# Optimization experiments

Measured on AMD Instinct MI355X. Metric: run time of the kernel, lower is better.

Reference implementation:

```python
import jax, jax.numpy as jnp
import numpy as np
import math

D_MODEL = 768
N_HEADS = 12
B, L = 2, 2048
ALPHA = 0.3

def setup_inputs() -> dict:
    key = jax.random.key(0)
    ks = jax.random.split(key, 7)
    s = 0.02
    return {
        "x": jax.random.normal(ks[0], (B, L, D_MODEL), dtype=jnp.float32),
        "Wqkv_w": jax.random.normal(ks[1], (D_MODEL, 3 * D_MODEL), dtype=jnp.float32) * s,
        "Wqkv_b": jax.random.normal(ks[2], (3 * D_MODEL,), dtype=jnp.float32) * s,
        "sel_w": jax.random.normal(ks[3], (D_MODEL, 2), dtype=jnp.float32) * s,
        "sel_b": jax.random.normal(ks[4], (2,), dtype=jnp.float32) * s,
        "out_w": jax.random.normal(ks[5], (D_MODEL, D_MODEL), dtype=jnp.float32) * s,
        "out_b": jax.random.normal(ks[6], (D_MODEL,), dtype=jnp.float32) * s,
        "temperature": jnp.ones((1,), dtype=jnp.float32) * (math.sqrt(D_MODEL) * ALPHA),
    }

def reference(x, Wqkv_w, Wqkv_b, sel_w, sel_b, out_w, out_b, temperature):
    b, l, d = x.shape
    h = N_HEADS
    hd = d // h
    # QKV projection: (B, L, 3, H, hd)
    qkv = (x @ Wqkv_w + Wqkv_b).reshape(b, l, 3, h, hd)
    q, k_, v = qkv[:, :, 0], qkv[:, :, 1], qkv[:, :, 2]
    scale = 1.0 / math.sqrt(hd)
    scores = jnp.einsum('bthd,bshd->bhts', q, k_ * scale)  # (B,H,L,L)
    causal_mask = jnp.triu(jnp.full((l, l), -10000.0, dtype=scores.dtype), 1)
    attn = jax.nn.softmax(scores + causal_mask, axis=-1)
    ctx = jnp.einsum('bhts,bshd->bthd', attn, v).reshape(b, l, d)
    attn_output = ctx @ out_w + out_b  # (B,L,D)
    # selection gate: softmax over 2 logits, keep prob of class 1 -> (B,L,1)
    selection = jax.nn.softmax((x @ sel_w + sel_b) / temperature, axis=-1)[..., 1:]
    # eval-mode top-k routing
    k_sel = int(math.ceil(math.sqrt(l)))
    _, idx = jax.lax.top_k(selection[..., 0], k_sel)  # (B, k)
    gated = attn_output * selection  # (B,L,D)
    src = jnp.take_along_axis(gated, idx[..., None], axis=1)  # (B,k,D)
    y = jax.vmap(lambda xb, ib, sb: xb.at[ib].add(sb))(x, idx, src)
    return y
```

## Files before the change

### kernel.cpp

```cpp
#include <hip/hip_runtime.h>
#include <hip/hip_bf16.h>
#include <cstddef>

#define BATCH 2
#define SEQ   2048
#define DM    768
#define NH    12
#define HD    64
#define N3    2304
#define NKV   1536
#define KSEL  46
#define NROW  (BATCH*KSEL)
#define NCHUNK 32

typedef unsigned short ushort_t;
typedef __attribute__((ext_vector_type(8))) short bf16x8;
typedef __attribute__((ext_vector_type(4))) float f32x4;

__device__ __forceinline__ ushort_t f2bf(float f) {
  union { __hip_bfloat16 h; ushort_t u; } cv;
  cv.h = __float2bfloat16(f);
  return cv.u;
}
__device__ __forceinline__ float bf2f(ushort_t u) {
  union { unsigned int i; float f; } cv;
  cv.i = ((unsigned int)u) << 16;
  return cv.f;
}

#define GLD16(g, l)                                                         \
  __builtin_amdgcn_global_load_lds(                                         \
      (const __attribute__((address_space(1))) void*)(g),                   \
      (__attribute__((address_space(3))) void*)(l), 16, 0, 0)

__global__ __launch_bounds__(256) void prep_kernel(
    const float* __restrict__ x, const float* __restrict__ W,
    const float* __restrict__ Wo,
    const float* __restrict__ sel_w, const float* __restrict__ sel_b,
    const float* __restrict__ temp,
    ushort_t* __restrict__ xb, ushort_t* __restrict__ Wt,
    ushort_t* __restrict__ WoT,
    float* __restrict__ sel, float* __restrict__ y) {
  const int bx = blockIdx.x;
  const int tid = threadIdx.x;
  if (bx < 3072) {
    int i = bx * 256 + tid;
    float4 f = ((const float4*)x)[i];
    ushort4 o;
    o.x = f2bf(f.x); o.y = f2bf(f.y); o.z = f2bf(f.z); o.w = f2bf(f.w);
    ((ushort4*)xb)[i] = o;
  } else if (bx < 4800) {
    __shared__ float tile[32][33];
    const int bx2 = bx - 3072;
    const int n0 = (bx2 % 72) * 32, k0 = (bx2 / 72) * 32;
    const int r = tid >> 3, c4 = (tid & 7) * 4;
    float4 f = *(const float4*)&W[(size_t)(k0 + r) * N3 + n0 + c4];
    tile[r][c4] = f.x; tile[r][c4 + 1] = f.y; tile[r][c4 + 2] = f.z; tile[r][c4 + 3] = f.w;
    __syncthreads();
    ushort4 o;
    o.x = f2bf(tile[c4 + 0][r]);
    o.y = f2bf(tile[c4 + 1][r]);
    o.z = f2bf(tile[c4 + 2][r]);
    o.w = f2bf(tile[c4 + 3][r]);
    *(ushort4*)&Wt[(size_t)(n0 + r) * DM + k0 + c4] = o;
  } else if (bx < 5376) {
    __shared__ float tile2[32][33];
    const int bx3 = bx - 4800;
    const int n0 = (bx3 % 24) * 32, k0 = (bx3 / 24) * 32;
    const int r = tid >> 3, c4 = (tid & 7) * 4;
    float4 f = *(const float4*)&Wo[(size_t)(k0 + r) * DM + n0 + c4];
    tile2[r][c4] = f.x; tile2[r][c4 + 1] = f.y; tile2[r][c4 + 2] = f.z; tile2[r][c4 + 3] = f.w;
    __syncthreads();
    ushort4 o;
    o.x = f2bf(tile2[c4 + 0][r]);
    o.y = f2bf(tile2[c4 + 1][r]);
    o.z = f2bf(tile2[c4 + 2][r]);
    o.w = f2bf(tile2[c4 + 3][r]);
    *(ushort4*)&WoT[(size_t)(n0 + r) * DM + k0 + c4] = o;
  } else if (bx < 6400) {
    int wave = tid >> 6, lane = tid & 63;
    int row = (bx - 5376) * 4 + wave;
    const float* xr = x + (size_t)row * DM;
    float a0 = 0.f, a1 = 0.f;
    for (int i = 0; i < DM / 64; ++i) {
      int k = lane + 64 * i;
      float xv = xr[k];
      a0 += xv * sel_w[2 * k];
      a1 += xv * sel_w[2 * k + 1];
    }
    for (int off = 32; off; off >>= 1) {
      a0 += __shfl_xor(a0, off);
      a1 += __shfl_xor(a1, off);
    }
    if (lane == 0) {
      float t = temp[0];
      float l0 = (a0 + sel_b[0]) / t;
      float l1 = (a1 + sel_b[1]) / t;
      sel[row] = 1.0f / (1.0f + expf(l0 - l1));
    }
  } else {
    int i = (bx - 6400) * 256 + tid;
    ((float4*)y)[i] = ((const float4*)x)[i];
  }
}

__global__ __launch_bounds__(256) void topk_kernel(
    const float* __restrict__ sel, int* __restrict__ idx,
    int* __restrict__ idxp) {
  __shared__ unsigned int hist[256];
  __shared__ unsigned int cum[256];
  __shared__ int sh_b;
  __shared__ int c_gt, c_eq;
  __shared__ int tmp_gt[KSEL];
  __shared__ int eqlist[256];
  const int b = blockIdx.x, tid = threadIdx.x;

  unsigned int key[8];
  int  kidx[8];
#pragma unroll
  for (int e = 0; e < 8; ++e) {
    int i = e * 256 + tid;
    kidx[e] = i;
    key[e] = __float_as_uint(sel[b * SEQ + i]);
  }
  unsigned int prefix = 0, mask = 0;
  int r = KSEL;
#pragma unroll
  for (int p = 3; p >= 0; --p) {
    const int shift = 8 * p;
    hist[tid] = 0;
    __syncthreads();
#pragma unroll
    for (int e = 0; e < 8; ++e)
      if ((key[e] & mask) == prefix)
        atomicAdd(&hist[(key[e] >> shift) & 255], 1u);
    __syncthreads();
    cum[tid] = hist[tid];
    __syncthreads();
    for (int d = 1; d < 256; d <<= 1) {
      unsigned int t = (tid + d < 256) ? cum[tid + d] : 0;
      __syncthreads();
      cum[tid] += t;
      __syncthreads();
    }
    if (cum[tid] >= (unsigned int)r && (tid == 255 || cum[tid + 1] < (unsigned int)r))
      sh_b = tid;
    __syncthreads();
    const int bsel = sh_b;
    r -= (bsel == 255) ? 0 : (int)cum[bsel + 1];
    prefix |= ((unsigned int)bsel) << shift;
    mask |= 0xFFu << shift;
    __syncthreads();
  }
  if (tid == 0) { c_gt = 0; c_eq = 0; }
  __syncthreads();
#pragma unroll
  for (int e = 0; e < 8; ++e) {
    if (key[e] > prefix) {
      int pos = atomicAdd(&c_gt, 1);
      tmp_gt[pos] = kidx[e];
    } else if (key[e] == prefix) {
      int pos = atomicAdd(&c_eq, 1);
      if (pos < 256) eqlist[pos] = kidx[e];
    }
  }
  __syncthreads();
  if (tid == 0) {
    const int need = KSEL - c_gt;
    const int ec = (c_eq < 256) ? c_eq : 256;
    for (int a = 0; a < need; ++a) {
      int mb = a;
      for (int bb = a + 1; bb < ec; ++bb)
        if (eqlist[bb] < eqlist[mb]) mb = bb;
      int tv = eqlist[a]; eqlist[a] = eqlist[mb]; eqlist[mb] = tv;
    }
  }
  __syncthreads();
  if (tid < 64) {
    if (tid < KSEL) {
      int t = (tid < c_gt) ? tmp_gt[tid] : eqlist[tid - c_gt];
      idx[b * KSEL + tid] = t;
      idxp[b * 64 + tid] = t;
    } else {
      idxp[b * 64 + tid] = 0;
    }
  }
}

__global__ __launch_bounds__(256) void gemm_kernel(
    const ushort_t* __restrict__ Xbf,
    const ushort_t* __restrict__ Wt,
    const float* __restrict__ bias,
    const int* __restrict__ idxp,
    ushort_t* __restrict__ Ckv,
    ushort_t* __restrict__ qb) {
  __shared__ ushort_t As[128 * 32];
  __shared__ ushort_t Bs[128 * 32];
  const int bid = blockIdx.x;
  const int tid = threadIdx.x;
  const int lane = tid & 63, w = tid >> 6;
  const int wr = w >> 1, wc = w & 1;
  const int quad = lane >> 4, l16 = lane & 15;
  const int ci0 = tid;
  const int ci1 = 256 + tid;
  const bool isQ = (bid >= 384);
  int m0, n0;
  size_t ga0, ga1;
  if (isQ) {
    m0 = 0;
    n0 = (bid - 384) * 128;
    const int r0 = ci0 >> 2, r1 = ci1 >> 2;
    ga0 = (size_t)((r0 >> 6) * SEQ + idxp[r0]) * DM;
    ga1 = (size_t)((r1 >> 6) * SEQ + idxp[r1]) * DM;
  } else {
    m0 = (bid / 12) * 128;
    n0 = 768 + (bid % 12) * 128;
    ga0 = (size_t)(m0 + (ci0 >> 2)) * DM;
    ga1 = (size_t)(m0 + (ci1 >> 2)) * DM;
  }
  const size_t gb0 = (size_t)(n0 + (ci0 >> 2)) * DM;
  const size_t gb1 = (size_t)(n0 + (ci1 >> 2)) * DM;
  const int ka0 = (ci0 & 3) * 8, ka1 = (ci1 & 3) * 8;

  f32x4 acc[4][4] = {};
  for (int k0 = 0; k0 < DM; k0 += 32) {
    GLD16(Xbf + ga0 + k0 + ka0, &As[(w * 64) * 8]);
    GLD16(Xbf + ga1 + k0 + ka1, &As[(256 + w * 64) * 8]);
    GLD16(Wt + gb0 + k0 + ka0, &Bs[(w * 64) * 8]);
    GLD16(Wt + gb1 + k0 + ka1, &Bs[(256 + w * 64) * 8]);
    __syncthreads();
    bf16x8 af[4], bfr[4];
#pragma unroll
    for (int i = 0; i < 4; ++i)
      af[i] = *(const bf16x8*)&As[(wr * 64 + i * 16 + l16) * 32 + quad * 8];
#pragma unroll
    for (int j = 0; j < 4; ++j)
      bfr[j] = *(const bf16x8*)&Bs[(wc * 64 + j * 16 + l16) * 32 + quad * 8];
#pragma unroll
    for (int i = 0; i < 4; ++i)
#pragma unroll
      for (int j = 0; j < 4; ++j)
        acc[i][j] = __builtin_amdgcn_mfma_f32_16x16x32_bf16(af[i], bfr[j], acc[i][j], 0, 0, 0);
    __syncthreads();
  }
#pragma unroll
  for (int i = 0; i < 4; ++i) {
    const int row_base = wr * 64 + i * 16 + quad * 4;
#pragma unroll
    for (int j = 0; j < 4; ++j) {
      const int col = n0 + wc * 64 + j * 16 + l16;
      const float bv = bias[col];
      if (isQ) {
#pragma unroll
        for (int r = 0; r < 4; ++r)
          qb[(size_t)(row_base + r) * DM + col] = f2bf(acc[i][j][r] + bv);
      } else {
#pragma unroll
        for (int r = 0; r < 4; ++r)
          Ckv[(size_t)(m0 + row_base + r) * NKV + (col - 768)] = f2bf(acc[i][j][r] + bv);
      }
    }
  }
}

__global__ __launch_bounds__(256) void attn_chunk_kernel(
    const ushort_t* __restrict__ kv,
    const ushort_t* __restrict__ qb,
    const int* __restrict__ idx,
    float* __restrict__ m_part, float* __restrict__ l_part,
    ushort_t* __restrict__ o_part) {
  __shared__ __align__(16) ushort_t Vt[64][72];
  __shared__ __align__(16) ushort_t Ps[4][16][72];
  __shared__ int tS[64];
  __shared__ int tmaxS;
  const int tid = threadIdx.x;
  const int c = blockIdx.x, h = blockIdx.y, b = blockIdx.z;
  const int c0 = c * 64;
  if (tid < 64) {
    int t = (tid < KSEL) ? idx[b * KSEL + tid] : -1;
    tS[tid] = t;
    int tm = t;
    for (int off = 32; off; off >>= 1) tm = max(tm, __shfl_xor(tm, off));
    if (tid == 0) tmaxS = tm;
  }
  __syncthreads();
  if (c0 > tmaxS) return;

  {
    const int key = tid >> 2, ds0 = (tid & 3) * 16;
    const ushort_t* vsrc = kv + (size_t)(b * SEQ + c0 + key) * NKV + DM + h * HD + ds0;
    ushort_t tmp[16];
    *(uint4*)&tmp[0] = *(const uint4*)&vsrc[0];
    *(uint4*)&tmp[8] = *(const uint4*)&vsrc[8];
#pragma unroll
    for (int i = 0; i < 16; ++i) Vt[ds0 + i][key] = tmp[i];
  }

  const int lane = tid & 63, w = tid >> 6;
  const int quad = lane >> 4, l16 = lane & 15;

  const ushort_t* qsrc = qb + (size_t)(b * 64 + w * 16 + l16) * DM + h * HD + quad * 8;
  bf16x8 aq0 = *(const bf16x8*)&qsrc[0];
  bf16x8 aq1 = *(const bf16x8*)&qsrc[32];

  f32x4 acc[4] = {};
#pragma unroll
  for (int nt = 0; nt < 4; ++nt) {
    const ushort_t* ksrc = kv + (size_t)(b * SEQ + c0 + nt * 16 + l16) * NKV + h * HD + quad * 8;
    bf16x8 bk0 = *(const bf16x8*)&ksrc[0];
    bf16x8 bk1 = *(const bf16x8*)&ksrc[32];
    acc[nt] = __builtin_amdgcn_mfma_f32_16x16x32_bf16(aq0, bk0, acc[nt], 0, 0, 0);
    acc[nt] = __builtin_amdgcn_mfma_f32_16x16x32_bf16(aq1, bk1, acc[nt], 0, 0, 0);
  }

  float p[4][4];
  float mrow[4], lrow[4];
#pragma unroll
  for (int r = 0; r < 4; ++r) {
    const int q = w * 16 + quad * 4 + r;
    const int t = tS[q];
    float mx = -1e30f;
#pragma unroll
    for (int nt = 0; nt < 4; ++nt) {
      float s = acc[nt][r] * 0.125f;
      if (c0 + nt * 16 + l16 > t) s = -1e30f;
      p[nt][r] = s;
      mx = fmaxf(mx, s);
    }
#pragma unroll
    for (int off = 1; off < 16; off <<= 1) mx = fmaxf(mx, __shfl_xor(mx, off));
    float sum = 0.f;
#pragma unroll
    for (int nt = 0; nt < 4; ++nt) {
      float pv = __expf(p[nt][r] - mx);
      p[nt][r] = pv;
      sum += pv;
    }
#pragma unroll
    for (int off = 1; off < 16; off <<= 1) sum += __shfl_xor(sum, off);
    mrow[r] = mx; lrow[r] = sum;
  }

  const size_t pbase = ((size_t)(b * NH + h) * NCHUNK + c) * 64;
  if (l16 == 0) {
#pragma unroll
    for (int r = 0; r < 4; ++r) {
      const int q = w * 16 + quad * 4 + r;
      m_part[pbase + q] = mrow[r];
      l_part[pbase + q] = lrow[r];
    }
  }

#pragma unroll
  for (int r = 0; r < 4; ++r)
#pragma unroll
    for (int nt = 0; nt < 4; ++nt)
      Ps[w][quad * 4 + r][nt * 16 + l16] = f2bf(p[nt][r]);
  __syncthreads();

  bf16x8 ap0 = *(const bf16x8*)&Ps[w][l16][quad * 8];
  bf16x8 ap1 = *(const bf16x8*)&Ps[w][l16][32 + quad * 8];
  f32x4 acc2[4] = {};
#pragma unroll
  for (int nt = 0; nt < 4; ++nt) {
    bf16x8 bv0 = *(const bf16x8*)&Vt[nt * 16 + l16][quad * 8];
    bf16x8 bv1 = *(const bf16x8*)&Vt[nt * 16 + l16][32 + quad * 8];
    acc2[nt] = __builtin_amdgcn_mfma_f32_16x16x32_bf16(ap0, bv0, acc2[nt], 0, 0, 0);
    acc2[nt] = __builtin_amdgcn_mfma_f32_16x16x32_bf16(ap1, bv1, acc2[nt], 0, 0, 0);
  }
  ushort_t* obp = o_part + pbase * 64;
#pragma unroll
  for (int nt = 0; nt < 4; ++nt)
#pragma unroll
    for (int r = 0; r < 4; ++r)
      obp[(w * 16 + quad * 4 + r) * 64 + nt * 16 + l16] = f2bf(acc2[nt][r]);
}

__global__ __launch_bounds__(256) void attn_combine_kernel(
    const float* __restrict__ m_part, const float* __restrict__ l_part,
    const ushort_t* __restrict__ o_part, const int* __restrict__ idx,
    ushort_t* __restrict__ ctx_bf) {
  __shared__ float wgt[NCHUNK][16];
  __shared__ float linv[16];
  __shared__ int ncS[16];
  const int rg = blockIdx.x, h = blockIdx.y, b = blockIdx.z;
  const int tid = threadIdx.x;
  const size_t base = (size_t)(b * NH + h) * NCHUNK * 64;
  if (tid < 16) {
    const int q = rg * 16 + tid;
    float L = 0.f; int nc = 0;
    if (q < KSEL) {
      const int t = idx[b * KSEL + q];
      nc = (t >> 6) + 1;
      float M = -1e30f;
      for (int cc = 0; cc < nc; ++cc)
        M = fmaxf(M, m_part[base + cc * 64 + q]);
      for (int cc = 0; cc < nc; ++cc) {
        float wv = __expf(m_part[base + cc * 64 + q] - M);
        wgt[cc][tid] = wv;
        L += wv * l_part[base + cc * 64 + q];
      }
    }
    ncS[tid] = nc;
    linv[tid] = (L > 0.f) ? 1.0f / L : 0.f;
  }
  __syncthreads();
  const int rl = tid >> 4;
  const int d4 = (tid & 15) * 4;
  const int q = rg * 16 + rl;
  if (q >= KSEL) return;
  const int nc = ncS[rl];
  float4 a = {0.f, 0.f, 0.f, 0.f};
  const ushort_t* obp = o_part + base * 64 + (size_t)q * 64 + d4;
  for (int cc = 0; cc < nc; ++cc) {
    const float wv = wgt[cc][rl];
    const ushort4 ov = *(const ushort4*)&obp[(size_t)cc * 4096];
    a.x += wv * bf2f(ov.x); a.y += wv * bf2f(ov.y);
    a.z += wv * bf2f(ov.z); a.w += wv * bf2f(ov.w);
  }
  const float li = linv[rl];
  ushort4 o;
  o.x = f2bf(a.x * li); o.y = f2bf(a.y * li);
  o.z = f2bf(a.z * li); o.w = f2bf(a.w * li);
  *(ushort4*)&ctx_bf[(size_t)(b * 64 + q) * DM + h * HD + d4] = o;
}

__global__ __launch_bounds__(256) void outproj_kernel(
    const ushort_t* __restrict__ ctx_bf,
    const ushort_t* __restrict__ WoT,
    const float* __restrict__ ob, const int* __restrict__ idx,
    const float* __restrict__ sel, float* __restrict__ y) {
  __shared__ ushort_t As[128 * 32];
  __shared__ ushort_t Bs[128 * 32];
  const int tid = threadIdx.x;
  const int lane = tid & 63, w = tid >> 6;
  const int wr = w >> 1, wc = w & 1;
  const int n0 = blockIdx.x * 128;
  const int quad = lane >> 4, l16 = lane & 15;
  const int ci0 = tid;
  const int ci1 = 256 + tid;
  const size_t ga0 = (size_t)(ci0 >> 2) * DM;
  const size_t ga1 = (size_t)(ci1 >> 2) * DM;
  const size_t gb0 = (size_t)(n0 + (ci0 >> 2)) * DM;
  const size_t gb1 = (size_t)(n0 + (ci1 >> 2)) * DM;
  const int ka0 = (ci0 & 3) * 8, ka1 = (ci1 & 3) * 8;
  f32x4 acc[4][4] = {};
  for (int k0 = 0; k0 < DM; k0 += 32) {
    GLD16(ctx_bf + ga0 + k0 + ka0, &As[(w * 64) * 8]);
    GLD16(ctx_bf + ga1 + k0 + ka1, &As[(256 + w * 64) * 8]);
    GLD16(WoT + gb0 + k0 + ka0, &Bs[(w * 64) * 8]);
    GLD16(WoT + gb1 + k0 + ka1, &Bs[(256 + w * 64) * 8]);
    __syncthreads();
    bf16x8 af[4], bfr[4];
#pragma unroll
    for (int i = 0; i < 4; ++i)
      af[i] = *(const bf16x8*)&As[(wr * 64 + i * 16 + l16) * 32 + quad * 8];
#pragma unroll
    for (int j = 0; j < 4; ++j)
      bfr[j] = *(const bf16x8*)&Bs[(wc * 64 + j * 16 + l16) * 32 + quad * 8];
#pragma unroll
    for (int i = 0; i < 4; ++i)
#pragma unroll
      for (int j = 0; j < 4; ++j)
        acc[i][j] = __builtin_amdgcn_mfma_f32_16x16x32_bf16(af[i], bfr[j], acc[i][j], 0, 0, 0);
    __syncthreads();
  }
#pragma unroll
  for (int i = 0; i < 4; ++i) {
#pragma unroll
    for (int r = 0; r < 4; ++r) {
      const int row = wr * 64 + i * 16 + quad * 4 + r;
      const int b = row >> 6, jj = row & 63;
      if (jj >= KSEL) continue;
      const int t = idx[b * KSEL + jj];
      const float sv = sel[b * SEQ + t];
      float* yr = y + (size_t)(b * SEQ + t) * DM;
#pragma unroll
      for (int j = 0; j < 4; ++j) {
        const int col = n0 + wc * 64 + j * 16 + l16;
        yr[col] += (acc[i][j][r] + ob[col]) * sv;
      }
    }
  }
}

extern "C" void kernel_launch(void* const* d_in, const int* in_sizes, int n_in,
                              void* d_out, int out_size, void* d_ws, size_t ws_size,
                              hipStream_t stream) {
  const float* x      = (const float*)d_in[0];
  const float* Wqkv_w = (const float*)d_in[1];
  const float* Wqkv_b = (const float*)d_in[2];
  const float* sel_w  = (const float*)d_in[3];
  const float* sel_b  = (const float*)d_in[4];
  const float* out_w  = (const float*)d_in[5];
  const float* out_b  = (const float*)d_in[6];
  const float* temp   = (const float*)d_in[7];
  float* y = (float*)d_out;

  char* wsb = (char*)d_ws;
  ushort_t* kv     = (ushort_t*)wsb;  wsb += (size_t)BATCH * SEQ * NKV * 2;
  ushort_t* o_part = (ushort_t*)wsb;  wsb += (size_t)24 * NCHUNK * 64 * 64 * 2;
  float*    m_part = (float*)wsb;     wsb += (size_t)24 * NCHUNK * 64 * 4;
  float*    l_part = (float*)wsb;     wsb += (size_t)24 * NCHUNK * 64 * 4;
  float*    sel    = (float*)wsb;     wsb += (size_t)BATCH * SEQ * 4;
  int*      idx    = (int*)wsb;       wsb += 128 * 4;
  int*      idxp   = (int*)wsb;       wsb += 128 * 4;
  ushort_t* ctx_bf = (ushort_t*)wsb;  wsb += (size_t)128 * DM * 2;
  ushort_t* qb     = (ushort_t*)wsb;  wsb += (size_t)128 * DM * 2;
  ushort_t* Xbf    = (ushort_t*)wsb;  wsb += (size_t)BATCH * SEQ * DM * 2;
  ushort_t* Wt     = (ushort_t*)wsb;  wsb += (size_t)N3 * DM * 2;
  ushort_t* WoT    = (ushort_t*)wsb;  wsb += (size_t)DM * DM * 2;

  prep_kernel<<<dim3(9472), 256, 0, stream>>>(x, Wqkv_w, out_w, sel_w, sel_b, temp,
                                              Xbf, Wt, WoT, sel, y);
  topk_kernel<<<dim3(BATCH), 256, 0, stream>>>(sel, idx, idxp);
  gemm_kernel<<<dim3(390), 256, 0, stream>>>(Xbf, Wt, Wqkv_b, idxp, kv, qb);
  attn_chunk_kernel<<<dim3(NCHUNK, NH, BATCH), 256, 0, stream>>>(kv, qb, idx, m_part, l_part, o_part);
  attn_combine_kernel<<<dim3(3, NH, BATCH), 256, 0, stream>>>(m_part, l_part, o_part, idx, ctx_bf);
  outproj_kernel<<<dim3(6), 256, 0, stream>>>(ctx_bf, WoT, out_b, idx, sel, y);
}
```

Baseline: 161.6 us.

## Fuse x passes in prep, wave-scan topk histogram, split-K outproj with atomics

The prep kernel now reads each x row once and, in the same pass, writes the bf16 copy, copies it into y and computes the selection gate dot product. This replaces three separate passes over x. The topk histogram prefix sum now uses wave shuffles plus a small per-wave total instead of a log-step shared-memory scan with many barriers. The output projection uses 64-wide N tiles and a 2-way K split, launching 24 blocks instead of 6, and accumulates into y with float atomics; the bias is added only by the first K half.

```diff
diff --git a/kernel.cpp b/kernel.cpp
--- a/kernel.cpp
+++ b/kernel.cpp
@@ -43,15 +43,40 @@
     float* __restrict__ sel, float* __restrict__ y) {
   const int bx = blockIdx.x;
   const int tid = threadIdx.x;
-  if (bx < 3072) {
-    int i = bx * 256 + tid;
-    float4 f = ((const float4*)x)[i];
-    ushort4 o;
-    o.x = f2bf(f.x); o.y = f2bf(f.y); o.z = f2bf(f.z); o.w = f2bf(f.w);
-    ((ushort4*)xb)[i] = o;
-  } else if (bx < 4800) {
+  if (bx < 1024) {
+    const int w = tid >> 6, lane = tid & 63;
+    const int row = bx * 4 + w;
+    const float4* xr4 = (const float4*)(x + (size_t)row * DM);
+    float4* yr4 = (float4*)(y + (size_t)row * DM);
+    ushort4* xb4 = (ushort4*)(xb + (size_t)row * DM);
+    const float4* sw4 = (const float4*)sel_w;
+    float a0 = 0.f, a1 = 0.f;
+#pragma unroll
+    for (int i = 0; i < 3; ++i) {
+      const int p = i * 64 + lane;
+      float4 f = xr4[p];
+      yr4[p] = f;
+      ushort4 o;
+      o.x = f2bf(f.x); o.y = f2bf(f.y); o.z = f2bf(f.z); o.w = f2bf(f.w);
+      xb4[p] = o;
+      float4 sa = sw4[p * 2];
+      float4 sb = sw4[p * 2 + 1];
+      a0 += f.x * sa.x + f.y * sa.z + f.z * sb.x + f.w * sb.z;
+      a1 += f.x * sa.y + f.y * sa.w + f.z * sb.y + f.w * sb.w;
+    }
+    for (int off = 32; off; off >>= 1) {
+      a0 += __shfl_xor(a0, off);
+      a1 += __shfl_xor(a1, off);
+    }
+    if (lane == 0) {
+      float t = temp[0];
+      float l0 = (a0 + sel_b[0]) / t;
+      float l1 = (a1 + sel_b[1]) / t;
+      sel[row] = 1.0f / (1.0f + expf(l0 - l1));
+    }
+  } else if (bx < 2752) {
     __shared__ float tile[32][33];
-    const int bx2 = bx - 3072;
+    const int bx2 = bx - 1024;
     const int n0 = (bx2 % 72) * 32, k0 = (bx2 / 72) * 32;
     const int r = tid >> 3, c4 = (tid & 7) * 4;
     float4 f = *(const float4*)&W[(size_t)(k0 + r) * N3 + n0 + c4];
@@ -63,9 +88,9 @@
     o.z = f2bf(tile[c4 + 2][r]);
     o.w = f2bf(tile[c4 + 3][r]);
     *(ushort4*)&Wt[(size_t)(n0 + r) * DM + k0 + c4] = o;
-  } else if (bx < 5376) {
+  } else {
     __shared__ float tile2[32][33];
-    const int bx3 = bx - 4800;
+    const int bx3 = bx - 2752;
     const int n0 = (bx3 % 24) * 32, k0 = (bx3 / 24) * 32;
     const int r = tid >> 3, c4 = (tid & 7) * 4;
     float4 f = *(const float4*)&Wo[(size_t)(k0 + r) * DM + n0 + c4];
@@ -77,30 +102,6 @@
     o.z = f2bf(tile2[c4 + 2][r]);
     o.w = f2bf(tile2[c4 + 3][r]);
     *(ushort4*)&WoT[(size_t)(n0 + r) * DM + k0 + c4] = o;
-  } else if (bx < 6400) {
-    int wave = tid >> 6, lane = tid & 63;
-    int row = (bx - 5376) * 4 + wave;
-    const float* xr = x + (size_t)row * DM;
-    float a0 = 0.f, a1 = 0.f;
-    for (int i = 0; i < DM / 64; ++i) {
-      int k = lane + 64 * i;
-      float xv = xr[k];
-      a0 += xv * sel_w[2 * k];
-      a1 += xv * sel_w[2 * k + 1];
-    }
-    for (int off = 32; off; off >>= 1) {
-      a0 += __shfl_xor(a0, off);
-      a1 += __shfl_xor(a1, off);
-    }
-    if (lane == 0) {
-      float t = temp[0];
-      float l0 = (a0 + sel_b[0]) / t;
-      float l1 = (a1 + sel_b[1]) / t;
-      sel[row] = 1.0f / (1.0f + expf(l0 - l1));
-    }
-  } else {
-    int i = (bx - 6400) * 256 + tid;
-    ((float4*)y)[i] = ((const float4*)x)[i];
   }
 }
 
@@ -109,11 +110,13 @@
     int* __restrict__ idxp) {
   __shared__ unsigned int hist[256];
   __shared__ unsigned int cum[256];
+  __shared__ unsigned int wtot[4];
   __shared__ int sh_b;
   __shared__ int c_gt, c_eq;
   __shared__ int tmp_gt[KSEL];
   __shared__ int eqlist[256];
   const int b = blockIdx.x, tid = threadIdx.x;
+  const int lane = tid & 63, w = tid >> 6;
 
   unsigned int key[8];
   int  kidx[8];
@@ -135,15 +138,20 @@
       if ((key[e] & mask) == prefix)
         atomicAdd(&hist[(key[e] >> shift) & 255], 1u);
     __syncthreads();
-    cum[tid] = hist[tid];
-    __syncthreads();
-    for (int d = 1; d < 256; d <<= 1) {
-      unsigned int t = (tid + d < 256) ? cum[tid + d] : 0;
-      __syncthreads();
-      cum[tid] += t;
-      __syncthreads();
-    }
-    if (cum[tid] >= (unsigned int)r && (tid == 255 || cum[tid + 1] < (unsigned int)r))
+    unsigned int v = hist[tid];
+#pragma unroll
+    for (int off = 1; off < 64; off <<= 1) {
+      unsigned int t = __shfl_down(v, off);
+      if (lane + off < 64) v += t;
+    }
+    if (lane == 0) wtot[w] = v;
+    __syncthreads();
+    unsigned int addhi = 0;
+    for (int ww = w + 1; ww < 4; ++ww) addhi += wtot[ww];
+    v += addhi;
+    cum[tid] = v;
+    __syncthreads();
+    if (v >= (unsigned int)r && (tid == 255 || cum[tid + 1] < (unsigned int)r))
       sh_b = tid;
     __syncthreads();
     const int bsel = sh_b;
@@ -431,37 +439,38 @@
     const float* __restrict__ ob, const int* __restrict__ idx,
     const float* __restrict__ sel, float* __restrict__ y) {
   __shared__ ushort_t As[128 * 32];
-  __shared__ ushort_t Bs[128 * 32];
+  __shared__ ushort_t Bs[64 * 32];
   const int tid = threadIdx.x;
   const int lane = tid & 63, w = tid >> 6;
   const int wr = w >> 1, wc = w & 1;
-  const int n0 = blockIdx.x * 128;
+  const int kb = blockIdx.x / 12;
+  const int n0 = (blockIdx.x % 12) * 64;
+  const int kbase = kb * 384;
   const int quad = lane >> 4, l16 = lane & 15;
   const int ci0 = tid;
   const int ci1 = 256 + tid;
   const size_t ga0 = (size_t)(ci0 >> 2) * DM;
   const size_t ga1 = (size_t)(ci1 >> 2) * DM;
-  const size_t gb0 = (size_t)(n0 + (ci0 >> 2)) * DM;
-  const size_t gb1 = (size_t)(n0 + (ci1 >> 2)) * DM;
+  const size_t gb0 = (size_t)(n0 + (tid >> 2)) * DM;
   const int ka0 = (ci0 & 3) * 8, ka1 = (ci1 & 3) * 8;
-  f32x4 acc[4][4] = {};
-  for (int k0 = 0; k0 < DM; k0 += 32) {
+  const int kq = (tid & 3) * 8;
+  f32x4 acc[4][2] = {};
+  for (int k0 = kbase; k0 < kbase + 384; k0 += 32) {
     GLD16(ctx_bf + ga0 + k0 + ka0, &As[(w * 64) * 8]);
     GLD16(ctx_bf + ga1 + k0 + ka1, &As[(256 + w * 64) * 8]);
-    GLD16(WoT + gb0 + k0 + ka0, &Bs[(w * 64) * 8]);
-    GLD16(WoT + gb1 + k0 + ka1, &Bs[(256 + w * 64) * 8]);
-    __syncthreads();
-    bf16x8 af[4], bfr[4];
+    GLD16(WoT + gb0 + k0 + kq, &Bs[(w * 16) * 32]);
+    __syncthreads();
+    bf16x8 af[4], bfr[2];
 #pragma unroll
     for (int i = 0; i < 4; ++i)
       af[i] = *(const bf16x8*)&As[(wr * 64 + i * 16 + l16) * 32 + quad * 8];
 #pragma unroll
-    for (int j = 0; j < 4; ++j)
-      bfr[j] = *(const bf16x8*)&Bs[(wc * 64 + j * 16 + l16) * 32 + quad * 8];
+    for (int j = 0; j < 2; ++j)
+      bfr[j] = *(const bf16x8*)&Bs[(wc * 32 + j * 16 + l16) * 32 + quad * 8];
 #pragma unroll
     for (int i = 0; i < 4; ++i)
 #pragma unroll
-      for (int j = 0; j < 4; ++j)
+      for (int j = 0; j < 2; ++j)
         acc[i][j] = __builtin_amdgcn_mfma_f32_16x16x32_bf16(af[i], bfr[j], acc[i][j], 0, 0, 0);
     __syncthreads();
   }
@@ -476,9 +485,10 @@
       const float sv = sel[b * SEQ + t];
       float* yr = y + (size_t)(b * SEQ + t) * DM;
 #pragma unroll
-      for (int j = 0; j < 4; ++j) {
-        const int col = n0 + wc * 64 + j * 16 + l16;
-        yr[col] += (acc[i][j][r] + ob[col]) * sv;
+      for (int j = 0; j < 2; ++j) {
+        const int col = n0 + wc * 32 + j * 16 + l16;
+        const float bv = (kb == 0) ? ob[col] : 0.f;
+        atomicAdd(&yr[col], (acc[i][j][r] + bv) * sv);
       }
     }
   }
@@ -511,11 +521,11 @@
   ushort_t* Wt     = (ushort_t*)wsb;  wsb += (size_t)N3 * DM * 2;
   ushort_t* WoT    = (ushort_t*)wsb;  wsb += (size_t)DM * DM * 2;
 
-  prep_kernel<<<dim3(9472), 256, 0, stream>>>(x, Wqkv_w, out_w, sel_w, sel_b, temp,
+  prep_kernel<<<dim3(3328), 256, 0, stream>>>(x, Wqkv_w, out_w, sel_w, sel_b, temp,
                                               Xbf, Wt, WoT, sel, y);
   topk_kernel<<<dim3(BATCH), 256, 0, stream>>>(sel, idx, idxp);
   gemm_kernel<<<dim3(390), 256, 0, stream>>>(Xbf, Wt, Wqkv_b, idxp, kv, qb);
   attn_chunk_kernel<<<dim3(NCHUNK, NH, BATCH), 256, 0, stream>>>(kv, qb, idx, m_part, l_part, o_part);
   attn_combine_kernel<<<dim3(3, NH, BATCH), 256, 0, stream>>>(m_part, l_part, o_part, idx, ctx_bf);
-  outproj_kernel<<<dim3(6), 256, 0, stream>>>(ctx_bf, WoT, out_b, idx, sel, y);
-}
+  outproj_kernel<<<dim3(24), 256, 0, stream>>>(ctx_bf, WoT, out_b, idx, sel, y);
+}
```

After: 154.8 us. 4.2% less time.
